# Performance work log

Measured on AMD Instinct MI355X. Metric: run time of the kernel, lower is better.

The kernel has to match this reference:

```python
import jax, jax.numpy as jnp
import numpy as np

B, S, E, H = 2, 2048, 1024, 16
HD = E // H
DFF = 4 * E
LN_EPS = 1e-5


def _layernorm(x, g, b):
    mu = jnp.mean(x, axis=-1, keepdims=True)
    var = jnp.mean(jnp.square(x - mu), axis=-1, keepdims=True)
    return (x - mu) * jax.lax.rsqrt(var + LN_EPS) * g + b


def setup_inputs() -> dict:
    key = jax.random.key(0)
    ks = jax.random.split(key, 6)
    inp = {
        "x": jax.random.normal(ks[0], (B, S, E), jnp.float32),
        "ln1_g": jnp.ones((E,), jnp.float32),
        "ln1_b": jnp.zeros((E,), jnp.float32),
        "ln2_g": jnp.ones((E,), jnp.float32),
        "ln2_b": jnp.zeros((E,), jnp.float32),
        # OptimizedPoincareBallLinear init: randn * 0.1, zero bias
        "w_qkv": jax.random.normal(ks[1], (3 * E, E), jnp.float32) * 0.1,
        "b_qkv": jnp.zeros((3 * E,), jnp.float32),
        "w_ao": jax.random.normal(ks[2], (E, E), jnp.float32) * 0.1,
        "b_ao": jnp.zeros((E,), jnp.float32),
        "w_fc": jax.random.normal(ks[3], (DFF, E), jnp.float32) * 0.1,
        "b_fc": jnp.zeros((DFF,), jnp.float32),
        "w_po": jax.random.normal(ks[4], (E, DFF), jnp.float32) * 0.1,
        "b_po": jnp.zeros((E,), jnp.float32),
    }
    return inp


def reference(x, ln1_g, ln1_b, ln2_g, ln2_b, w_qkv, b_qkv, w_ao, b_ao,
              w_fc, b_fc, w_po, b_po):
    # --- attention branch ---
    h = _layernorm(x, ln1_g, ln1_b)
    qkv = h @ w_qkv.T + b_qkv                       # [B,S,3E]
    qkv = qkv.reshape(B, S, H, 3 * HD).transpose(0, 2, 1, 3)  # [B,H,S,3hd]
    q, k, v = jnp.split(qkv, 3, axis=-1)            # each [B,H,S,hd]
    scores = jnp.einsum('bhqd,bhkd->bhqk', q, k) / jnp.sqrt(
        jnp.asarray(HD, jnp.float32))
    causal = jnp.tril(jnp.ones((S, S), bool))        # attn_bias[:, :, :S, :S]
    scores = jnp.where(causal, scores, jnp.finfo(scores.dtype).min)
    attn_w = jax.nn.softmax(scores, axis=-1)         # dropout p=0.1 inactive (eval)
    attn = jnp.einsum('bhqk,bhkd->bhqd', attn_w, v)  # [B,H,S,hd]
    attn = attn.transpose(0, 2, 1, 3).reshape(B, S, E)
    attn = attn @ w_ao.T + b_ao
    x = x + attn
    # --- MLP branch ---
    h2 = _layernorm(x, ln2_g, ln2_b)
    h2 = h2 @ w_fc.T + b_fc
    h2 = jax.nn.gelu(h2, approximate=True)           # GPT-2 gelu_new
    h2 = h2 @ w_po.T + b_po
    x = x + h2
    return x
```

## Files before the change

kernel.cpp:

```cpp
#include <hip/hip_runtime.h>
#include <cstddef>
#include <cstdint>

#define Bc 2
#define Sc 2048
#define Ec 1024
#define Hc 16
#define HDc 64
#define DFFc 4096
#define ROWS (Bc * Sc)

typedef _Float16 half8v __attribute__((ext_vector_type(8)));
typedef _Float16 half4v __attribute__((ext_vector_type(4)));
typedef float f32x4 __attribute__((ext_vector_type(4)));
typedef _Float16 h16;

__device__ inline void gld_lds16(const void* g, void* l) {
    __builtin_amdgcn_global_load_lds(
        (const __attribute__((address_space(1))) void*)g,
        (__attribute__((address_space(3))) void*)l, 16, 0, 0);
}

__device__ inline float gelu_new(float x) {
    float x2 = x * x;
    float u = x * fmaf(0.07135481627362f, x2, 1.5957691216057308f);
    return x / (1.0f + __expf(-u));
}

__global__ __launch_bounds__(256) void cvt4_kernel(
    const float* __restrict__ a,
    const float* __restrict__ b,
    const float* __restrict__ c,
    const float* __restrict__ d,
    h16* __restrict__ out)
{
    int bid = blockIdx.x;
    const float* src;
    size_t obase;
    int base;
    if (bid < 3072)      { src = a; obase = 0;       base = bid; }
    else if (bid < 4096) { src = b; obase = 3145728; base = bid - 3072; }
    else if (bid < 8192) { src = c; obase = 4194304; base = bid - 4096; }
    else                 { src = d; obase = 8388608; base = bid - 8192; }
    int i = base * 1024 + threadIdx.x * 4;
    float4 v = *(const float4*)(src + i);
    half4v o;
    o.x = (h16)v.x; o.y = (h16)v.y; o.z = (h16)v.z; o.w = (h16)v.w;
    *(half4v*)(out + obase + i) = o;
}

__device__ inline float block_sum256(float v, float* sb) {
    #pragma unroll
    for (int o = 32; o > 0; o >>= 1) v += __shfl_down(v, o, 64);
    int lane = threadIdx.x & 63, w = threadIdx.x >> 6;
    if (lane == 0) sb[w] = v;
    __syncthreads();
    float r = sb[0] + sb[1] + sb[2] + sb[3];
    __syncthreads();
    return r;
}

__global__ __launch_bounds__(256) void ln_kernel(const float* __restrict__ x,
                                                 const float* __restrict__ g,
                                                 const float* __restrict__ b,
                                                 h16* __restrict__ out) {
    __shared__ float sb[4];
    int row = blockIdx.x;
    int t = threadIdx.x;
    const float* xr = x + (size_t)row * Ec;
    float4 v = ((const float4*)xr)[t];
    float s = v.x + v.y + v.z + v.w;
    float mu = block_sum256(s, sb) * (1.0f / Ec);
    float dx = v.x - mu, dy = v.y - mu, dz = v.z - mu, dw = v.w - mu;
    float ss = dx * dx + dy * dy + dz * dz + dw * dw;
    float var = block_sum256(ss, sb) * (1.0f / Ec);
    float inv = rsqrtf(var + 1e-5f);
    float4 gv = ((const float4*)g)[t];
    float4 bv = ((const float4*)b)[t];
    half4v o;
    o.x = (h16)(dx * inv * gv.x + bv.x);
    o.y = (h16)(dy * inv * gv.y + bv.y);
    o.z = (h16)(dz * inv * gv.z + bv.z);
    o.w = (h16)(dw * inv * gv.w + bv.w);
    ((half4v*)(out + (size_t)row * Ec))[t] = o;
}

template <int EPI, typename OutT>
__global__ __launch_bounds__(512, 2) void gemm_8w(
    const h16* __restrict__ A, const h16* __restrict__ W,
    const float* __restrict__ bias, const float* __restrict__ R,
    OutT* __restrict__ C, int M, int N, int K)
{
    __shared__ h16 S[4][16384];

    const int tid = threadIdx.x;
    const int lane = tid & 63, wv = tid >> 6;
    const int wm = wv >> 2, wn = wv & 3;
    const int c15 = lane & 15, q = lane >> 4;

    const int nbn = N >> 8;
    const int cpx = gridDim.x >> 3;
    const int wg = ((int)blockIdx.x & 7) * cpx + ((int)blockIdx.x >> 3);
    const int r0 = (wg / nbn) << 8, c0 = (wg % nbn) << 8;

    const int gc8 = (tid & 3) ^ ((tid >> 3) & 3);
    const h16* gA = A + (size_t)(r0 + (tid >> 2)) * K + gc8 * 8;
    const h16* gB = W + (size_t)(c0 + (tid >> 2)) * K + gc8 * 8;
    const size_t hK = (size_t)128 * K;

    int aoff[8], boff[4];
    #pragma unroll
    for (int m = 0; m < 8; ++m) {
        int row = wm * 128 + m * 16 + c15;
        aoff[m] = row * 32 + ((q ^ ((row >> 1) & 3)) << 3);
    }
    #pragma unroll
    for (int n = 0; n < 4; ++n) {
        int row = wn * 64 + n * 16 + c15;
        boff[n] = 8192 + row * 32 + ((q ^ ((row >> 1) & 3)) << 3);
    }

    f32x4 acc[8][4];
    #pragma unroll
    for (int m = 0; m < 8; ++m)
        #pragma unroll
        for (int n = 0; n < 4; ++n)
            acc[m][n] = (f32x4){0.f, 0.f, 0.f, 0.f};

    const int NT = K >> 5;

    auto stage = [&](int tt) {
        h16* b = &S[tt & 3][0];
        const h16* a = gA + tt * 32;
        const h16* w = gB + tt * 32;
        gld_lds16(a,      b + tid * 8);
        gld_lds16(a + hK, b + 4096 + tid * 8);
        gld_lds16(w,      b + 8192 + tid * 8);
        gld_lds16(w + hK, b + 12288 + tid * 8);
    };

    stage(0); stage(1); stage(2);
    asm volatile("s_waitcnt vmcnt(8)" ::: "memory");
    __builtin_amdgcn_s_barrier();

    for (int t = 0; t < NT; ++t) {
        if (t + 3 < NT) stage(t + 3);

        const h16* b = &S[t & 3][0];
        half8v af[8], bf[4];
        #pragma unroll
        for (int m = 0; m < 8; ++m) af[m] = *(const half8v*)(b + aoff[m]);
        #pragma unroll
        for (int n = 0; n < 4; ++n) bf[n] = *(const half8v*)(b + boff[n]);

        __builtin_amdgcn_s_setprio(1);
        #pragma unroll
        for (int m = 0; m < 8; ++m)
            #pragma unroll
            for (int n = 0; n < 4; ++n)
                acc[m][n] = __builtin_amdgcn_mfma_f32_16x16x32_f16(af[m], bf[n], acc[m][n], 0, 0, 0);
        __builtin_amdgcn_s_setprio(0);

        if (t < NT - 1) {
            if (t + 3 < NT)       asm volatile("s_waitcnt vmcnt(8)" ::: "memory");
            else if (t + 3 == NT) asm volatile("s_waitcnt vmcnt(4)" ::: "memory");
            else                  asm volatile("s_waitcnt vmcnt(0)" ::: "memory");
            __builtin_amdgcn_s_barrier();
        }
    }

    float bvs[4];
    #pragma unroll
    for (int n = 0; n < 4; ++n) bvs[n] = bias[c0 + wn * 64 + n * 16 + c15];
    #pragma unroll
    for (int m = 0; m < 8; ++m) {
        #pragma unroll
        for (int n = 0; n < 4; ++n) {
            int col = c0 + wn * 64 + n * 16 + c15;
            #pragma unroll
            for (int r = 0; r < 4; ++r) {
                int row = r0 + wm * 128 + m * 16 + q * 4 + r;
                size_t off = (size_t)row * N + col;
                float v = acc[m][n][r] + bvs[n];
                if (EPI == 1) v += R[off];
                if (EPI == 2) v = gelu_new(v);
                if (sizeof(OutT) == 2) ((h16*)C)[off] = (h16)v;
                else ((float*)C)[off] = v;
            }
        }
    }
}

template <int EPI, typename OutT>
__global__ __launch_bounds__(256, 2) void gemm_k64(
    const h16* __restrict__ A, const h16* __restrict__ W,
    const float* __restrict__ bias, const float* __restrict__ R,
    OutT* __restrict__ C, int M, int N, int K)
{
    __shared__ h16 S[4][6144];

    const int t = threadIdx.x;
    const int lane = t & 63, wv = t >> 6;
    const int wm = wv >> 1, wn = wv & 1;
    const int c15 = lane & 15, q = lane >> 4;
    const int id = blockIdx.x;
    const int cx = id & 7;
    const int kq = id >> 3;
    const int bx = kq & 7;
    const int by = ((kq >> 3) << 3) | cx;
    const int row0 = by * 64, col0 = bx * 128;

    const int gc8 = (t & 3) ^ ((t >> 3) & 3);
    const h16* gA  = A + (size_t)(row0 + (t >> 2)) * K + gc8 * 8;
    const h16* gB0 = W + (size_t)(col0 + (t >> 2)) * K + gc8 * 8;
    const h16* gB1 = gB0 + (size_t)64 * K;

    int aoff[2], boff[4];
    #pragma unroll
    for (int i = 0; i < 2; ++i) {
        int row = wm * 32 + i * 16 + c15;
        aoff[i] = row * 32 + ((q ^ ((row >> 1) & 3)) << 3);
    }
    #pragma unroll
    for (int j = 0; j < 4; ++j) {
        int row = wn * 64 + j * 16 + c15;
        boff[j] = 2048 + row * 32 + ((q ^ ((row >> 1) & 3)) << 3);
    }

    f32x4 acc[2][4];
    #pragma unroll
    for (int i = 0; i < 2; ++i)
        #pragma unroll
        for (int j = 0; j < 4; ++j)
            acc[i][j] = (f32x4){0.f, 0.f, 0.f, 0.f};

    const int NT = K >> 5;

    auto stage = [&](int tt) {
        h16* b = &S[tt & 3][0];
        gld_lds16(gA  + tt * 32, b + t * 8);
        gld_lds16(gB0 + tt * 32, b + 2048 + t * 8);
        gld_lds16(gB1 + tt * 32, b + 4096 + t * 8);
    };

    stage(0); stage(1); stage(2);
    asm volatile("s_waitcnt vmcnt(6)" ::: "memory");
    __builtin_amdgcn_s_barrier();

    for (int tt = 0; tt < NT; ++tt) {
        if (tt + 3 < NT) stage(tt + 3);

        const h16* b = &S[tt & 3][0];
        half8v af[2], bf[4];
        #pragma unroll
        for (int i = 0; i < 2; ++i) af[i] = *(const half8v*)(b + aoff[i]);
        #pragma unroll
        for (int j = 0; j < 4; ++j) bf[j] = *(const half8v*)(b + boff[j]);

        __builtin_amdgcn_s_setprio(1);
        #pragma unroll
        for (int i = 0; i < 2; ++i)
            #pragma unroll
            for (int j = 0; j < 4; ++j)
                acc[i][j] = __builtin_amdgcn_mfma_f32_16x16x32_f16(af[i], bf[j], acc[i][j], 0, 0, 0);
        __builtin_amdgcn_s_setprio(0);

        if (tt < NT - 1) {
            if (tt + 3 < NT)       asm volatile("s_waitcnt vmcnt(6)" ::: "memory");
            else if (tt + 3 == NT) asm volatile("s_waitcnt vmcnt(3)" ::: "memory");
            else                   asm volatile("s_waitcnt vmcnt(0)" ::: "memory");
            __builtin_amdgcn_s_barrier();
        }
    }

    #pragma unroll
    for (int i = 0; i < 2; ++i) {
        #pragma unroll
        for (int j = 0; j < 4; ++j) {
            int col = col0 + wn * 64 + j * 16 + c15;
            float bv = bias[col];
            #pragma unroll
            for (int r = 0; r < 4; ++r) {
                int row = row0 + wm * 32 + i * 16 + q * 4 + r;
                size_t off = (size_t)row * N + col;
                float v = acc[i][j][r] + bv;
                if (EPI == 1) v += R[off];
                if (EPI == 2) v = gelu_new(v);
                if (sizeof(OutT) == 2) ((h16*)C)[off] = (h16)v;
                else ((float*)C)[off] = v;
            }
        }
    }
}

__global__ __launch_bounds__(256, 4) void attn_mfma(const h16* __restrict__ qkv,
                                                    h16* __restrict__ attn) {
    __shared__ h16 Ks[2][2][64 * 32];
    __shared__ h16 Vt[2][64 * 32];
    __shared__ h16 Ps[4][16 * 72];

    const int t = threadIdx.x;
    const int lane = t & 63, wv = t >> 6;
    const int c15 = lane & 15, q = lane >> 4;
    const int bh = blockIdx.x, b = bh >> 4, h = bh & 15;
    const int ja = 31 - blockIdx.y;
    const int qbase = ja * 64 + wv * 16;
    const int SE = 3 * Ec;
    const size_t hbase = (size_t)b * Sc * SE + (size_t)h * (3 * HDc);

    half8v qf[2];
    #pragma unroll
    for (int kk = 0; kk < 2; ++kk) {
        qf[kk] = *(const half8v*)(qkv + hbase + (size_t)(qbase + c15) * SE + kk * 32 + q * 8);
        qf[kk] *= (h16)0.125f;
    }

    f32x4 O[4];
    #pragma unroll
    for (int n = 0; n < 4; ++n) O[n] = (f32x4){0.f, 0.f, 0.f, 0.f};
    float mi = -3e38f, li = 0.f;

    const int krow = t >> 2, kcol = (t & 3) << 3;
    const int vkey = t & 31, vd0 = (t >> 5) << 3;
    half8v vreg[2];

    auto stageK = [&](int kt, int bf) {
        #pragma unroll
        for (int p = 0; p < 2; ++p)
            gld_lds16(qkv + hbase + (size_t)(kt * 64 + krow) * SE + HDc + p * 32 + kcol,
                      &Ks[bf][p][krow * 32 + kcol]);
    };
    auto loadV = [&](int kt) {
        #pragma unroll
        for (int p = 0; p < 2; ++p)
            vreg[p] = *(const half8v*)(qkv + hbase +
                        (size_t)(kt * 64 + p * 32 + vkey) * SE + 2 * HDc + vd0);
    };
    auto scatV = [&]() {
        #pragma unroll
        for (int p = 0; p < 2; ++p)
            #pragma unroll
            for (int u = 0; u < 8; ++u)
                Vt[p][(vd0 + u) * 32 + vkey] = vreg[p][u];
    };

    stageK(0, 0);
    loadV(0);
    scatV();
    __syncthreads();

    for (int kt = 0; kt <= ja; ++kt) {
        const int bf = kt & 1;
        if (kt < ja) { stageK(kt + 1, bf ^ 1); loadV(kt + 1); }

        f32x4 st[4];
        #pragma unroll
        for (int j = 0; j < 4; ++j) {
            half8v kf0 = *(const half8v*)&Ks[bf][0][(j * 16 + c15) * 32 + q * 8];
            half8v kf1 = *(const half8v*)&Ks[bf][1][(j * 16 + c15) * 32 + q * 8];
            f32x4 z = (f32x4){0.f, 0.f, 0.f, 0.f};
            z = __builtin_amdgcn_mfma_f32_16x16x32_f16(kf0, qf[0], z, 0, 0, 0);
            st[j] = __builtin_amdgcn_mfma_f32_16x16x32_f16(kf1, qf[1], z, 0, 0, 0);
        }

        if (kt == ja) {
            const int rowloc = wv * 16 + c15;
            #pragma unroll
            for (int j = 0; j < 4; ++j)
                #pragma unroll
                for (int r = 0; r < 4; ++r)
                    if (j * 16 + q * 4 + r > rowloc) st[j][r] = -3e38f;
        }

        float mx = mi;
        #pragma unroll
        for (int j = 0; j < 4; ++j)
            #pragma unroll
            for (int r = 0; r < 4; ++r) mx = fmaxf(mx, st[j][r]);
        mx = fmaxf(mx, __shfl_xor(mx, 16, 64));
        mx = fmaxf(mx, __shfl_xor(mx, 32, 64));
        float al = __expf(mi - mx);
        mi = mx;
        float ps = 0.f;
        #pragma unroll
        for (int j = 0; j < 4; ++j) {
            half4v pk;
            #pragma unroll
            for (int r = 0; r < 4; ++r) {
                float p = __expf(st[j][r] - mx);
                ps += p;
                pk[r] = (h16)p;
            }
            *(half4v*)&Ps[wv][c15 * 72 + j * 16 + q * 4] = pk;
        }
        ps += __shfl_xor(ps, 16, 64);
        ps += __shfl_xor(ps, 32, 64);
        li = li * al + ps;

        half8v pb0 = *(const half8v*)&Ps[wv][c15 * 72 + q * 8];
        half8v pb1 = *(const half8v*)&Ps[wv][c15 * 72 + 32 + q * 8];
        #pragma unroll
        for (int n = 0; n < 4; ++n) {
            #pragma unroll
            for (int r = 0; r < 4; ++r) O[n][r] *= al;
            half8v va0 = *(const half8v*)&Vt[0][(n * 16 + c15) * 32 + q * 8];
            half8v va1 = *(const half8v*)&Vt[1][(n * 16 + c15) * 32 + q * 8];
            O[n] = __builtin_amdgcn_mfma_f32_16x16x32_f16(va0, pb0, O[n], 0, 0, 0);
            O[n] = __builtin_amdgcn_mfma_f32_16x16x32_f16(va1, pb1, O[n], 0, 0, 0);
        }

        if (kt < ja) {
            __syncthreads();
            scatV();
            __syncthreads();
        }
    }

    float rl = 1.0f / li;
    #pragma unroll
    for (int n = 0; n < 4; ++n) {
        half4v o4;
        #pragma unroll
        for (int r = 0; r < 4; ++r) o4[r] = (h16)(O[n][r] * rl);
        *(half4v*)(attn + ((size_t)(b * Sc + qbase + c15)) * Ec + h * HDc + n * 16 + q * 4) = o4;
    }
}

extern "C" void kernel_launch(void* const* d_in, const int* in_sizes, int n_in,
                              void* d_out, int out_size, void* d_ws, size_t ws_size,
                              hipStream_t stream) {
    const float* x     = (const float*)d_in[0];
    const float* ln1_g = (const float*)d_in[1];
    const float* ln1_b = (const float*)d_in[2];
    const float* ln2_g = (const float*)d_in[3];
    const float* ln2_b = (const float*)d_in[4];
    const float* w_qkv = (const float*)d_in[5];
    const float* b_qkv = (const float*)d_in[6];
    const float* w_ao  = (const float*)d_in[7];
    const float* b_ao  = (const float*)d_in[8];
    const float* w_fc  = (const float*)d_in[9];
    const float* b_fc  = (const float*)d_in[10];
    const float* w_po  = (const float*)d_in[11];
    const float* b_po  = (const float*)d_in[12];
    float* out = (float*)d_out;

    char* w = (char*)d_ws;
    h16* wqkv = (h16*)(w);
    h16* wao  = (h16*)(w + 6291456);
    h16* wfc  = (h16*)(w + 8388608);
    h16* wpo  = (h16*)(w + 16777216);
    h16* hb   = (h16*)(w + 25165824);
    h16* qkv  = (h16*)(w + 33554432);
    h16* attn = (h16*)(w + 58720256);
    float* x1 = (float*)(w + 67108864);
    h16* ff   = qkv;

    dim3 blk(256);
    dim3 blk8(512);

    cvt4_kernel<<<dim3(12288), blk, 0, stream>>>(w_qkv, w_ao, w_fc, w_po, wqkv);

    ln_kernel<<<dim3(ROWS), blk, 0, stream>>>(x, ln1_g, ln1_b, hb);
    gemm_8w<0, h16><<<dim3((ROWS / 256) * (3 * Ec / 256)), blk8, 0, stream>>>(
        hb, wqkv, b_qkv, nullptr, qkv, ROWS, 3 * Ec, Ec);
    attn_mfma<<<dim3(Bc * Hc, 32), blk, 0, stream>>>(qkv, attn);
    gemm_k64<1, float><<<dim3(512), blk, 0, stream>>>(
        attn, wao, b_ao, x, x1, ROWS, Ec, Ec);
    ln_kernel<<<dim3(ROWS), blk, 0, stream>>>(x1, ln2_g, ln2_b, hb);
    gemm_8w<2, h16><<<dim3((ROWS / 256) * (DFFc / 256)), blk8, 0, stream>>>(
        hb, wfc, b_fc, nullptr, ff, ROWS, DFFc, Ec);
    gemm_k64<1, float><<<dim3(512), blk, 0, stream>>>(
        ff, wpo, b_po, x1, out, ROWS, Ec, DFFc);
}
```

Before: 348.3 us.

## Split-K the MLP output projection over the 8-wave GEMM with a reduction kernel

The final K=4096 projection GEMM now runs on the 256x256-tile 8-wave kernel, split into four K=1024 slices, giving 256 workgroups. Three slices write fp16 partial sums into workspace regions that are dead by then (the qkv/ao weights, the fc weights and the LN buffer). The fourth slice writes fp32 directly to the output. A new elementwise kernel then adds the three partials, the residual and the bias into the output. The aim is a more efficient large-tile MFMA path and full-device occupancy for this GEMM. The cost is extra partial-sum memory traffic, an extra launch, and precision loss from storing partials in fp16.

```diff
diff --git a/kernel.cpp b/kernel.cpp
--- a/kernel.cpp
+++ b/kernel.cpp
@@ -89,7 +89,7 @@
 __global__ __launch_bounds__(512, 2) void gemm_8w(
     const h16* __restrict__ A, const h16* __restrict__ W,
     const float* __restrict__ bias, const float* __restrict__ R,
-    OutT* __restrict__ C, int M, int N, int K)
+    OutT* __restrict__ C, int M, int N, int K, int lda)
 {
     __shared__ h16 S[4][16384];
 
@@ -98,15 +98,24 @@
     const int wm = wv >> 2, wn = wv & 3;
     const int c15 = lane & 15, q = lane >> 4;
 
-    const int nbn = N >> 8;
     const int cpx = gridDim.x >> 3;
     const int wg = ((int)blockIdx.x & 7) * cpx + ((int)blockIdx.x >> 3);
-    const int r0 = (wg / nbn) << 8, c0 = (wg % nbn) << 8;
+    int r0, c0, sp = 0;
+    if (EPI == 3) {
+        sp = wg >> 6;
+        int rem = wg & 63;
+        r0 = (rem >> 2) << 8;
+        c0 = (rem & 3) << 8;
+    } else {
+        const int nbn = N >> 8;
+        r0 = (wg / nbn) << 8;
+        c0 = (wg % nbn) << 8;
+    }
 
     const int gc8 = (tid & 3) ^ ((tid >> 3) & 3);
-    const h16* gA = A + (size_t)(r0 + (tid >> 2)) * K + gc8 * 8;
-    const h16* gB = W + (size_t)(c0 + (tid >> 2)) * K + gc8 * 8;
-    const size_t hK = (size_t)128 * K;
+    const h16* gA = A + (size_t)(r0 + (tid >> 2)) * lda + sp * 1024 + gc8 * 8;
+    const h16* gB = W + (size_t)(c0 + (tid >> 2)) * lda + sp * 1024 + gc8 * 8;
+    const size_t hK = (size_t)128 * lda;
 
     int aoff[8], boff[4];
     #pragma unroll
@@ -169,6 +178,11 @@
         }
     }
 
+    h16* Pp = nullptr;
+    if (EPI == 3 && sp < 3) {
+        size_t po = (sp == 0) ? 0 : (sp == 1) ? 8388608u : 25165824u;
+        Pp = (h16*)((char*)(void*)R + po);
+    }
     float bvs[4];
     #pragma unroll
     for (int n = 0; n < 4; ++n) bvs[n] = bias[c0 + wn * 64 + n * 16 + c15];
@@ -181,14 +195,52 @@
             for (int r = 0; r < 4; ++r) {
                 int row = r0 + wm * 128 + m * 16 + q * 4 + r;
                 size_t off = (size_t)row * N + col;
-                float v = acc[m][n][r] + bvs[n];
-                if (EPI == 1) v += R[off];
-                if (EPI == 2) v = gelu_new(v);
-                if (sizeof(OutT) == 2) ((h16*)C)[off] = (h16)v;
-                else ((float*)C)[off] = v;
+                if (EPI == 3) {
+                    float v = acc[m][n][r];
+                    if (sp < 3) Pp[off] = (h16)v;
+                    else ((float*)C)[off] = v;
+                } else {
+                    float v = acc[m][n][r] + bvs[n];
+                    if (EPI == 1) v += R[off];
+                    if (EPI == 2) v = gelu_new(v);
+                    if (sizeof(OutT) == 2) ((h16*)C)[off] = (h16)v;
+                    else ((float*)C)[off] = v;
+                }
             }
         }
     }
+}
+
+__global__ __launch_bounds__(256) void red3_kernel(
+    const h16* __restrict__ P0, const h16* __restrict__ P1,
+    const h16* __restrict__ P2, const float* __restrict__ xr,
+    const float* __restrict__ bias, float* __restrict__ out)
+{
+    size_t i = ((size_t)blockIdx.x * 256 + threadIdx.x) * 8;
+    int col = (int)(i & 1023);
+    half8v p0 = *(const half8v*)(P0 + i);
+    half8v p1 = *(const half8v*)(P1 + i);
+    half8v p2 = *(const half8v*)(P2 + i);
+    float4 x0 = *(const float4*)(xr + i);
+    float4 x1v = *(const float4*)(xr + i + 4);
+    float4 b0 = *(const float4*)(bias + col);
+    float4 b1 = *(const float4*)(bias + col + 4);
+    float4 o0 = *(const float4*)(out + i);
+    float4 o1 = *(const float4*)(out + i + 4);
+    float ps[8];
+    #pragma unroll
+    for (int u = 0; u < 8; ++u)
+        ps[u] = (float)p0[u] + (float)p1[u] + (float)p2[u];
+    o0.x += x0.x + b0.x + ps[0];
+    o0.y += x0.y + b0.y + ps[1];
+    o0.z += x0.z + b0.z + ps[2];
+    o0.w += x0.w + b0.w + ps[3];
+    o1.x += x1v.x + b1.x + ps[4];
+    o1.y += x1v.y + b1.y + ps[5];
+    o1.z += x1v.z + b1.z + ps[6];
+    o1.w += x1v.w + b1.w + ps[7];
+    *(float4*)(out + i) = o0;
+    *(float4*)(out + i + 4) = o1;
 }
 
 template <int EPI, typename OutT>
@@ -462,13 +514,16 @@
 
     ln_kernel<<<dim3(ROWS), blk, 0, stream>>>(x, ln1_g, ln1_b, hb);
     gemm_8w<0, h16><<<dim3((ROWS / 256) * (3 * Ec / 256)), blk8, 0, stream>>>(
-        hb, wqkv, b_qkv, nullptr, qkv, ROWS, 3 * Ec, Ec);
+        hb, wqkv, b_qkv, nullptr, qkv, ROWS, 3 * Ec, Ec, Ec);
     attn_mfma<<<dim3(Bc * Hc, 32), blk, 0, stream>>>(qkv, attn);
     gemm_k64<1, float><<<dim3(512), blk, 0, stream>>>(
         attn, wao, b_ao, x, x1, ROWS, Ec, Ec);
     ln_kernel<<<dim3(ROWS), blk, 0, stream>>>(x1, ln2_g, ln2_b, hb);
     gemm_8w<2, h16><<<dim3((ROWS / 256) * (DFFc / 256)), blk8, 0, stream>>>(
-        hb, wfc, b_fc, nullptr, ff, ROWS, DFFc, Ec);
-    gemm_k64<1, float><<<dim3(512), blk, 0, stream>>>(
-        ff, wpo, b_po, x1, out, ROWS, Ec, DFFc);
-}
+        hb, wfc, b_fc, nullptr, ff, ROWS, DFFc, Ec, Ec);
+    gemm_8w<3, float><<<dim3(256), blk8, 0, stream>>>(
+        ff, wpo, b_po, (const float*)w, out, ROWS, Ec, 1024, DFFc);
+    red3_kernel<<<dim3(2048), blk, 0, stream>>>(
+        (const h16*)w, (const h16*)(w + 8388608), (const h16*)(w + 25165824),
+        x1, b_po, out);
+}
```

Result: faster. 324.2 us (-6.9%).
